# Kernel tuning notes

Measured on AMD Instinct MI355X. Metric: run time of the kernel, lower is better.

Reference implementation:

```python
import jax, jax.numpy as jnp
import numpy as np

POS_HALF = 4   # positive window: [t-4, t+4)
NEG_LEN = 12   # negatives: up to 12 frames on each side of the positive window
K_MAX = 2 * POS_HALF + 2 * NEG_LEN  # 32 candidates max per timestep


def _build_windows(T):
    """Static [T,K_MAX] gather indices + positive/valid masks (numpy, trace-time)."""
    idx = np.zeros((T, K_MAX), np.int32)
    pos_mask = np.zeros((T, K_MAX), bool)
    valid = np.zeros((T, K_MAX), bool)
    for t in range(T):
        start, end = max(0, t - POS_HALF), min(T, t + POS_HALF)
        pos = list(range(start, end))
        neg = list(range(max(0, start - NEG_LEN), start)) + \
              list(range(end, min(T, end + NEG_LEN)))
        comb = pos + neg
        idx[t, :len(comb)] = comb
        valid[t, :len(comb)] = True
        pos_mask[t, :len(pos)] = True
    return jnp.asarray(idx), jnp.asarray(pos_mask), jnp.asarray(valid)


def _directional(q, kv, idx, pos_mask, valid, scale, bias):
    # q, kv: [B,T,D] (L2-normalized); idx/pos_mask/valid: [T,K]
    w = kv[:, idx]  # [B,T,K,D] windowed gather
    logits = jnp.einsum('btd,btkd->btk', q, w) * scale + bias  # [B,T,K]
    sign = jnp.where(pos_mask, 1.0, -1.0)
    loglik = jax.nn.log_sigmoid(sign * logits)
    # per-t: sum over window, mean over batch; then sum over t
    loss = -jnp.where(valid, loglik, 0.0).sum(axis=2).mean(axis=0).sum()
    am = jnp.argmax(jnp.where(valid, logits, -jnp.inf), axis=2)  # [B,T]
    T = q.shape[1]
    correct = pos_mask[jnp.arange(T)[None, :], am].astype(jnp.float32).sum()
    return loss, correct


def setup_inputs() -> dict:
    key = jax.random.key(0)
    k1, k2 = jax.random.split(key)
    B, T, D = 8, 1024, 512
    return {
        "motion_feature": jax.random.normal(k1, (B, T, D), jnp.float32),
        "audio_feature": jax.random.normal(k2, (B, T, D), jnp.float32),
        "logit_scale": jnp.asarray(np.log(1.0 / 0.07), jnp.float32),  # param (pre-exp)
        "logit_bias": jnp.asarray(0.0, jnp.float32),                  # param
    }


def reference(motion_feature, audio_feature, logit_scale, logit_bias):
    B, T, _ = motion_feature.shape
    eps = 1e-12
    m = motion_feature / jnp.clip(
        jnp.linalg.norm(motion_feature, axis=2, keepdims=True), eps)
    a = audio_feature / jnp.clip(
        jnp.linalg.norm(audio_feature, axis=2, keepdims=True), eps)
    scale = jnp.exp(logit_scale)
    idx, pos_mask, valid = _build_windows(T)
    m2a_loss, m2a_correct = _directional(m, a, idx, pos_mask, valid, scale, logit_bias)
    a2m_loss, a2m_correct = _directional(a, m, idx, pos_mask, valid, scale, logit_bias)
    final_loss = (m2a_loss + a2m_loss) / (2 * T)
    total_correct = (m2a_correct + a2m_correct) / (2 * T * B)
    return final_loss, total_correct
```

## Files before the change

kernel.cpp:

```cpp
#include <hip/hip_runtime.h>
#include <hip/hip_bf16.h>
#include <math.h>

#define B_DIM 8
#define T_DIM 1024
#define D_DIM 512
#define BT (B_DIM * T_DIM)
#define NBLK 512

typedef __bf16 bf16x8 __attribute__((ext_vector_type(8)));
typedef float floatx4 __attribute__((ext_vector_type(4)));

__device__ __forceinline__ float wave_reduce_sum(float v) {
#pragma unroll
    for (int off = 32; off > 0; off >>= 1) v += __shfl_xor(v, off, 64);
    return v;
}

__device__ __forceinline__ float softplus(float y) {
    return fmaxf(y, 0.0f) + log1pf(expf(-fabsf(y)));
}

__device__ __forceinline__ bf16x8 cvt8(float4 x, float4 y) {
    union { ushort u[8]; bf16x8 v; } r;
    __hip_bfloat162 h0 = __float22bfloat162_rn(make_float2(x.x, x.y));
    __hip_bfloat162 h1 = __float22bfloat162_rn(make_float2(x.z, x.w));
    __hip_bfloat162 h2 = __float22bfloat162_rn(make_float2(y.x, y.y));
    __hip_bfloat162 h3 = __float22bfloat162_rn(make_float2(y.z, y.w));
    ushort2 p0 = *(ushort2*)&h0, p1 = *(ushort2*)&h1;
    ushort2 p2 = *(ushort2*)&h2, p3 = *(ushort2*)&h3;
    r.u[0] = p0.x; r.u[1] = p0.y; r.u[2] = p1.x; r.u[3] = p1.y;
    r.u[4] = p2.x; r.u[5] = p2.y; r.u[6] = p3.x; r.u[7] = p3.y;
    return r.v;
}

__global__ __launch_bounds__(512, 4) void crossband_kernel(
    const float* __restrict__ m, const float* __restrict__ a,
    const float* __restrict__ pscale, const float* __restrict__ pbias,
    float* __restrict__ part_loss, float* __restrict__ part_corr)
{
    __shared__ float red[8][5][272];
    __shared__ float Sbuf[48][49];
    __shared__ float red2[8][6][16];
    __shared__ float norms[6][16];
    __shared__ float rowpos[16], colpos[16], shl[8];

    int blk = blockIdx.x;
    int b   = blk >> 6;
    int t0  = (blk & 63) << 4;
    int tid  = threadIdx.x;
    int w    = tid >> 6;
    int lane = tid & 63;
    int mrow = lane & 15;
    int kgrp = lane >> 4;
    int koff = w * 64 + kgrp * 8;

    const float* mb = m + ((size_t)b << 19);
    const float* ab = a + ((size_t)b << 19);

    const float* mp[3]; const float* ap[3];
#pragma unroll
    for (int s = 0; s < 3; ++s) {
        int r = t0 - 16 + s * 16 + mrow;
        r = min(max(r, 0), T_DIM - 1);
        mp[s] = mb + (size_t)r * D_DIM + koff;
        ap[s] = ab + (size_t)r * D_DIM + koff;
    }

    floatx4 acc[5];
#pragma unroll
    for (int q = 0; q < 5; ++q) acc[q] = (floatx4){0.f,0.f,0.f,0.f};
    float ssm[3] = {0.f,0.f,0.f}, ssa[3] = {0.f,0.f,0.f};

#pragma unroll
    for (int ks = 0; ks < 2; ++ks) {
        bf16x8 am[3], av[3];
#pragma unroll
        for (int s = 0; s < 3; ++s) {
            float4 x = *(const float4*)(mp[s] + ks * 32);
            float4 y = *(const float4*)(mp[s] + ks * 32 + 4);
            ssm[s] += x.x*x.x + x.y*x.y + x.z*x.z + x.w*x.w
                    + y.x*y.x + y.y*y.y + y.z*y.z + y.w*y.w;
            am[s] = cvt8(x, y);
            float4 u = *(const float4*)(ap[s] + ks * 32);
            float4 v = *(const float4*)(ap[s] + ks * 32 + 4);
            ssa[s] += u.x*u.x + u.y*u.y + u.z*u.z + u.w*u.w
                    + v.x*v.x + v.y*v.y + v.z*v.z + v.w*v.w;
            av[s] = cvt8(u, v);
        }
        acc[0] = __builtin_amdgcn_mfma_f32_16x16x32_bf16(am[1], av[0], acc[0], 0, 0, 0);
        acc[1] = __builtin_amdgcn_mfma_f32_16x16x32_bf16(am[1], av[1], acc[1], 0, 0, 0);
        acc[2] = __builtin_amdgcn_mfma_f32_16x16x32_bf16(am[1], av[2], acc[2], 0, 0, 0);
        acc[3] = __builtin_amdgcn_mfma_f32_16x16x32_bf16(am[0], av[1], acc[3], 0, 0, 0);
        acc[4] = __builtin_amdgcn_mfma_f32_16x16x32_bf16(am[2], av[1], acc[4], 0, 0, 0);
    }

#pragma unroll
    for (int off = 16; off <= 32; off <<= 1) {
#pragma unroll
        for (int s = 0; s < 3; ++s) {
            ssm[s] += __shfl_xor(ssm[s], off, 64);
            ssa[s] += __shfl_xor(ssa[s], off, 64);
        }
    }
    if (kgrp == 0) {
#pragma unroll
        for (int s = 0; s < 3; ++s) {
            red2[w][s][mrow]     = ssm[s];
            red2[w][3 + s][mrow] = ssa[s];
        }
    }
#pragma unroll
    for (int q = 0; q < 5; ++q)
#pragma unroll
        for (int r = 0; r < 4; ++r)
            red[w][q][(kgrp * 4 + r) * 17 + mrow] = acc[q][r];
    __syncthreads();

    if (tid < 96) {
        int slot = tid >> 4, mr = tid & 15;
        float ss = 0.f;
#pragma unroll
        for (int ww = 0; ww < 8; ++ww) ss += red2[ww][slot][mr];
        norms[slot][mr] = 1.0f / fmaxf(sqrtf(ss), 1e-12f);
    }
    {
        const int tu[5] = {16, 16, 16, 0, 32};
        const int tv[5] = {0, 16, 32, 16, 16};
#pragma unroll
        for (int e = 0; e < 3; ++e) {
            int idx = tid + e * 512;
            if (idx < 1280) {
                int q = idx >> 8, r2 = idx & 255;
                int rho = r2 >> 4, kap = r2 & 15;
                float s4 = 0.f;
#pragma unroll
                for (int ww = 0; ww < 8; ++ww)
                    s4 += red[ww][q][rho * 17 + kap];
                Sbuf[tu[q] + rho][tv[q] + kap] = s4;
            }
        }
    }
    __syncthreads();

    float scale = expf(pscale[0]), bias = pbias[0];
    float loss = 0.0f;

    if (tid < 256) {
        int i = tid >> 4, cc = tid & 15;
        float im_u = norms[1][i];
        float mmax = -1e30f, mpos = 0.0f;
#pragma unroll
        for (int tj = 0; tj < 3; ++tj) {
            int v  = tj * 16 + cc;
            int dd = v - i;
            int c  = t0 - 16 + v;
            if (dd >= 0 && dd < 32 && c >= 0 && c < T_DIM) {
                float sv = Sbuf[16 + i][v] * norms[3 + tj][cc];
                float logit = sv * im_u * scale + bias;
                bool pos = (dd >= 12) && (dd <= 19);
                loss += softplus(pos ? -logit : logit);
                if (sv > mmax) { mmax = sv; mpos = pos ? 1.0f : 0.0f; }
            }
        }
#pragma unroll
        for (int off = 1; off < 16; off <<= 1) {
            float ov = __shfl_xor(mmax, off, 64);
            float op = __shfl_xor(mpos, off, 64);
            if (ov > mmax) { mmax = ov; mpos = op; }
        }
        if (cc == 0) rowpos[i] = mpos;
    } else {
        int t2 = tid - 256;
        int i = t2 >> 4, cc = t2 & 15;
        float ia_v = norms[4][i];
        float amax = -1e30f, apos = 0.0f;
#pragma unroll
        for (int tj = 0; tj < 3; ++tj) {
            int u2 = tj * 16 + cc;
            int ee = u2 - i;
            int r  = t0 - 16 + u2;
            if (ee >= 0 && ee < 32 && r >= 0 && r < T_DIM) {
                float sv = Sbuf[u2][16 + i] * norms[tj][cc];
                float logit = sv * ia_v * scale + bias;
                bool pos = (ee >= 12) && (ee <= 19);
                loss += softplus(pos ? -logit : logit);
                if (sv > amax) { amax = sv; apos = pos ? 1.0f : 0.0f; }
            }
        }
#pragma unroll
        for (int off = 1; off < 16; off <<= 1) {
            float ov = __shfl_xor(amax, off, 64);
            float op = __shfl_xor(apos, off, 64);
            if (ov > amax) { amax = ov; apos = op; }
        }
        if (cc == 0) colpos[i] = apos;
    }

    loss = wave_reduce_sum(loss);
    if (lane == 0) shl[w] = loss;
    __syncthreads();
    if (tid == 0) {
        float L = 0.0f, C = 0.0f;
#pragma unroll
        for (int r = 0; r < 8; ++r) L += shl[r];
#pragma unroll
        for (int r = 0; r < 16; ++r) C += rowpos[r] + colpos[r];
        part_loss[blk] = L;
        part_corr[blk] = C;
    }
}

__global__ __launch_bounds__(256) void finalsum_kernel(
    const float* __restrict__ part_loss, const float* __restrict__ part_corr,
    float* __restrict__ out)
{
    int tid = threadIdx.x;
    float l = part_loss[tid] + part_loss[tid + 256];
    float c = part_corr[tid] + part_corr[tid + 256];
    l = wave_reduce_sum(l);
    c = wave_reduce_sum(c);
    __shared__ float shl[4], shc[4];
    int w = tid >> 6, lane = tid & 63;
    if (lane == 0) { shl[w] = l; shc[w] = c; }
    __syncthreads();
    if (tid == 0) {
        out[0] = (shl[0] + shl[1] + shl[2] + shl[3]) / 16384.0f;
        out[1] = (shc[0] + shc[1] + shc[2] + shc[3]) / 16384.0f;
    }
}

extern "C" void kernel_launch(void* const* d_in, const int* in_sizes, int n_in,
                              void* d_out, int out_size, void* d_ws, size_t ws_size,
                              hipStream_t stream)
{
    const float* m  = (const float*)d_in[0];
    const float* a  = (const float*)d_in[1];
    const float* ps = (const float*)d_in[2];
    const float* pb = (const float*)d_in[3];
    float* out = (float*)d_out;

    float* part_loss = (float*)d_ws;
    float* part_corr = part_loss + NBLK;

    crossband_kernel<<<NBLK, 512, 0, stream>>>(m, a, ps, pb, part_loss, part_corr);
    finalsum_kernel<<<1, 256, 0, stream>>>(part_loss, part_corr, out);
}
```

Baseline: 90.72 us.

## Split band kernel into per-wave MFMA kernel and separate epilogue reduction kernel

The single fused kernel, where each 512-thread block reduced eight waves' partial MFMA tiles through shared memory, is replaced by two kernels. The first runs independent waves (four per 256-thread block) that write their partial dot-product tiles and squared norms to global workspace. The second kernel sums those partials, normalises, and computes the loss and argmax. Softplus also switches to fast __expf/__logf intrinsics. This trades an extra launch and about 21 MB of global partial traffic for smaller blocks and no shared-memory cross-wave reduction in the load phase.

```diff
diff --git a/kernel.cpp b/kernel.cpp
--- a/kernel.cpp
+++ b/kernel.cpp
@@ -6,7 +6,11 @@
 #define T_DIM 1024
 #define D_DIM 512
 #define BT (B_DIM * T_DIM)
-#define NBLK 512
+#define NTILES 512
+#define WPT 8
+#define NWAVES (NTILES * WPT)
+#define PART_STRIDE 1280
+#define SS_STRIDE 96
 
 typedef __bf16 bf16x8 __attribute__((ext_vector_type(8)));
 typedef float floatx4 __attribute__((ext_vector_type(4)));
@@ -18,7 +22,7 @@
 }
 
 __device__ __forceinline__ float softplus(float y) {
-    return fmaxf(y, 0.0f) + log1pf(expf(-fabsf(y)));
+    return fmaxf(y, 0.0f) + __logf(1.0f + __expf(-fabsf(y)));
 }
 
 __device__ __forceinline__ bf16x8 cvt8(float4 x, float4 y) {
@@ -34,23 +38,16 @@
     return r.v;
 }
 
-__global__ __launch_bounds__(512, 4) void crossband_kernel(
+__global__ __launch_bounds__(256, 4) void band2_kernel(
     const float* __restrict__ m, const float* __restrict__ a,
-    const float* __restrict__ pscale, const float* __restrict__ pbias,
-    float* __restrict__ part_loss, float* __restrict__ part_corr)
-{
-    __shared__ float red[8][5][272];
-    __shared__ float Sbuf[48][49];
-    __shared__ float red2[8][6][16];
-    __shared__ float norms[6][16];
-    __shared__ float rowpos[16], colpos[16], shl[8];
-
-    int blk = blockIdx.x;
-    int b   = blk >> 6;
-    int t0  = (blk & 63) << 4;
-    int tid  = threadIdx.x;
-    int w    = tid >> 6;
-    int lane = tid & 63;
+    float* __restrict__ part, float* __restrict__ ssbuf)
+{
+    int wg   = blockIdx.x * 4 + (threadIdx.x >> 6);
+    int tile = wg >> 3;
+    int w    = wg & 7;
+    int b    = tile >> 6;
+    int t0   = (tile & 63) << 4;
+    int lane = threadIdx.x & 63;
     int mrow = lane & 15;
     int kgrp = lane >> 4;
     int koff = w * 64 + kgrp * 8;
@@ -104,50 +101,65 @@
         }
     }
     if (kgrp == 0) {
+        float* sw = ssbuf + (size_t)wg * SS_STRIDE;
 #pragma unroll
         for (int s = 0; s < 3; ++s) {
-            red2[w][s][mrow]     = ssm[s];
-            red2[w][3 + s][mrow] = ssa[s];
-        }
-    }
+            sw[s * 16 + mrow]       = ssm[s];
+            sw[(3 + s) * 16 + mrow] = ssa[s];
+        }
+    }
+    float* pw = part + (size_t)wg * PART_STRIDE;
 #pragma unroll
     for (int q = 0; q < 5; ++q)
 #pragma unroll
         for (int r = 0; r < 4; ++r)
-            red[w][q][(kgrp * 4 + r) * 17 + mrow] = acc[q][r];
+            pw[q * 256 + (kgrp * 4 + r) * 16 + mrow] = acc[q][r];
+}
+
+__global__ __launch_bounds__(256) void epi_kernel(
+    const float* __restrict__ part, const float* __restrict__ ssbuf,
+    const float* __restrict__ pscale, const float* __restrict__ pbias,
+    float* __restrict__ part_loss, float* __restrict__ part_corr)
+{
+    __shared__ float Sbuf[48][49];
+    __shared__ float norms[6][16];
+    __shared__ float rowpos[16], colpos[16], shl[4];
+
+    int tile = blockIdx.x;
+    int t0   = (tile & 63) << 4;
+    int tid  = threadIdx.x;
+    int w    = tid >> 6;
+    int lane = tid & 63;
+
+    float scale = expf(pscale[0]), bias = pbias[0];
+
+    const float* pbase = part + (size_t)tile * WPT * PART_STRIDE;
+    const int tu[5] = {16, 16, 16, 0, 32};
+    const int tv[5] = {0, 16, 32, 16, 16};
+#pragma unroll
+    for (int j = 0; j < 5; ++j) {
+        int e = tid + j * 256;
+        float s = 0.f;
+#pragma unroll
+        for (int wgi = 0; wgi < WPT; ++wgi)
+            s += pbase[wgi * PART_STRIDE + e];
+        int q = e >> 8, r2 = e & 255;
+        Sbuf[tu[q] + (r2 >> 4)][tv[q] + (r2 & 15)] = s;
+    }
+    if (tid < 96) {
+        const float* sbase = ssbuf + (size_t)tile * WPT * SS_STRIDE;
+        float ss = 0.f;
+#pragma unroll
+        for (int wgi = 0; wgi < WPT; ++wgi)
+            ss += sbase[wgi * SS_STRIDE + tid];
+        norms[tid >> 4][tid & 15] = 1.0f / fmaxf(sqrtf(ss), 1e-12f);
+    }
     __syncthreads();
 
-    if (tid < 96) {
-        int slot = tid >> 4, mr = tid & 15;
-        float ss = 0.f;
-#pragma unroll
-        for (int ww = 0; ww < 8; ++ww) ss += red2[ww][slot][mr];
-        norms[slot][mr] = 1.0f / fmaxf(sqrtf(ss), 1e-12f);
-    }
+    int i = tid >> 4, cc = tid & 15;
+    float loss = 0.0f;
+
     {
-        const int tu[5] = {16, 16, 16, 0, 32};
-        const int tv[5] = {0, 16, 32, 16, 16};
-#pragma unroll
-        for (int e = 0; e < 3; ++e) {
-            int idx = tid + e * 512;
-            if (idx < 1280) {
-                int q = idx >> 8, r2 = idx & 255;
-                int rho = r2 >> 4, kap = r2 & 15;
-                float s4 = 0.f;
-#pragma unroll
-                for (int ww = 0; ww < 8; ++ww)
-                    s4 += red[ww][q][rho * 17 + kap];
-                Sbuf[tu[q] + rho][tv[q] + kap] = s4;
-            }
-        }
-    }
-    __syncthreads();
-
-    float scale = expf(pscale[0]), bias = pbias[0];
-    float loss = 0.0f;
-
-    if (tid < 256) {
-        int i = tid >> 4, cc = tid & 15;
         float im_u = norms[1][i];
         float mmax = -1e30f, mpos = 0.0f;
 #pragma unroll
@@ -170,9 +182,8 @@
             if (ov > mmax) { mmax = ov; mpos = op; }
         }
         if (cc == 0) rowpos[i] = mpos;
-    } else {
-        int t2 = tid - 256;
-        int i = t2 >> 4, cc = t2 & 15;
+    }
+    {
         float ia_v = norms[4][i];
         float amax = -1e30f, apos = 0.0f;
 #pragma unroll
@@ -201,13 +212,11 @@
     if (lane == 0) shl[w] = loss;
     __syncthreads();
     if (tid == 0) {
-        float L = 0.0f, C = 0.0f;
-#pragma unroll
-        for (int r = 0; r < 8; ++r) L += shl[r];
+        float C = 0.0f;
 #pragma unroll
         for (int r = 0; r < 16; ++r) C += rowpos[r] + colpos[r];
-        part_loss[blk] = L;
-        part_corr[blk] = C;
+        part_loss[tile] = shl[0] + shl[1] + shl[2] + shl[3];
+        part_corr[tile] = C;
     }
 }
 
@@ -240,9 +249,13 @@
     const float* pb = (const float*)d_in[3];
     float* out = (float*)d_out;
 
-    float* part_loss = (float*)d_ws;
-    float* part_corr = part_loss + NBLK;
-
-    crossband_kernel<<<NBLK, 512, 0, stream>>>(m, a, ps, pb, part_loss, part_corr);
+    float* part      = (float*)d_ws;
+    float* ssbuf     = part + (size_t)NWAVES * PART_STRIDE;
+    float* part_loss = ssbuf + (size_t)NWAVES * SS_STRIDE;
+    float* part_corr = part_loss + NTILES;
+
+    band2_kernel<<<NWAVES / 4, 256, 0, stream>>>(m, a, part, ssbuf);
+    epi_kernel<<<NTILES, 256, 0, stream>>>(part, ssbuf, ps, pb,
+                                           part_loss, part_corr);
     finalsum_kernel<<<1, 256, 0, stream>>>(part_loss, part_corr, out);
 }
```

New measurement: 98.37 us. +8.4%, slower.

## Split normalization and bf16 conversion into a prep kernel before banded MFMA

Applied to the files above, without the earlier changes.

Adds a prep kernel that L2-normalizes each row of both inputs and writes bf16 copies to workspace. The banded MFMA kernel then reads these bf16 rows, about half the bytes, and no longer computes norms, so its per-block norm reductions go away. Blocks shrink to 256 threads, each wave covering more of K, and the block order is interleaved across the batch. The cost is an extra launch plus a full fp32 read and bf16 write-then-read round trip through workspace, while the old single kernel read each fp32 row about three times from cache.

```diff
diff --git a/kernel.cpp b/kernel.cpp
--- a/kernel.cpp
+++ b/kernel.cpp
@@ -1,5 +1,4 @@
 #include <hip/hip_runtime.h>
-#include <hip/hip_bf16.h>
 #include <math.h>
 
 #define B_DIM 8
@@ -17,48 +16,67 @@
     return v;
 }
 
+__device__ __forceinline__ ushort f2bf(float x) {
+    unsigned u = __float_as_uint(x);
+    return (ushort)((u + 0x7fffu + ((u >> 16) & 1u)) >> 16);
+}
+
 __device__ __forceinline__ float softplus(float y) {
     return fmaxf(y, 0.0f) + log1pf(expf(-fabsf(y)));
 }
 
-__device__ __forceinline__ bf16x8 cvt8(float4 x, float4 y) {
-    union { ushort u[8]; bf16x8 v; } r;
-    __hip_bfloat162 h0 = __float22bfloat162_rn(make_float2(x.x, x.y));
-    __hip_bfloat162 h1 = __float22bfloat162_rn(make_float2(x.z, x.w));
-    __hip_bfloat162 h2 = __float22bfloat162_rn(make_float2(y.x, y.y));
-    __hip_bfloat162 h3 = __float22bfloat162_rn(make_float2(y.z, y.w));
-    ushort2 p0 = *(ushort2*)&h0, p1 = *(ushort2*)&h1;
-    ushort2 p2 = *(ushort2*)&h2, p3 = *(ushort2*)&h3;
-    r.u[0] = p0.x; r.u[1] = p0.y; r.u[2] = p1.x; r.u[3] = p1.y;
-    r.u[4] = p2.x; r.u[5] = p2.y; r.u[6] = p3.x; r.u[7] = p3.y;
-    return r.v;
-}
-
-__global__ __launch_bounds__(512, 4) void crossband_kernel(
+__global__ __launch_bounds__(256) void prep_kernel(
     const float* __restrict__ m, const float* __restrict__ a,
+    ushort* __restrict__ mhat, ushort* __restrict__ ahat)
+{
+    int blk = blockIdx.x;
+    int wid = (blk & 7) * 1024 + (blk >> 3) * 4 + (threadIdx.x >> 6);
+    int lane = threadIdx.x & 63;
+    const float4* mr = (const float4*)(m + (size_t)wid * D_DIM);
+    const float4* ar = (const float4*)(a + (size_t)wid * D_DIM);
+    float4 m0 = mr[lane], m1 = mr[lane + 64];
+    float4 a0 = ar[lane], a1 = ar[lane + 64];
+    float sm = m0.x*m0.x + m0.y*m0.y + m0.z*m0.z + m0.w*m0.w
+             + m1.x*m1.x + m1.y*m1.y + m1.z*m1.z + m1.w*m1.w;
+    float sa = a0.x*a0.x + a0.y*a0.y + a0.z*a0.z + a0.w*a0.w
+             + a1.x*a1.x + a1.y*a1.y + a1.z*a1.z + a1.w*a1.w;
+    sm = wave_reduce_sum(sm);
+    sa = wave_reduce_sum(sa);
+    float im = 1.0f / fmaxf(sqrtf(sm), 1e-12f);
+    float ia = 1.0f / fmaxf(sqrtf(sa), 1e-12f);
+    ushort4 mo0 = { f2bf(m0.x*im), f2bf(m0.y*im), f2bf(m0.z*im), f2bf(m0.w*im) };
+    ushort4 mo1 = { f2bf(m1.x*im), f2bf(m1.y*im), f2bf(m1.z*im), f2bf(m1.w*im) };
+    ushort4 ao0 = { f2bf(a0.x*ia), f2bf(a0.y*ia), f2bf(a0.z*ia), f2bf(a0.w*ia) };
+    ushort4 ao1 = { f2bf(a1.x*ia), f2bf(a1.y*ia), f2bf(a1.z*ia), f2bf(a1.w*ia) };
+    ushort4* mw = (ushort4*)(mhat + (size_t)wid * D_DIM);
+    ushort4* aw = (ushort4*)(ahat + (size_t)wid * D_DIM);
+    mw[lane] = mo0; mw[lane + 64] = mo1;
+    aw[lane] = ao0; aw[lane + 64] = ao1;
+}
+
+__global__ __launch_bounds__(256) void crossband_kernel(
+    const ushort* __restrict__ mhat, const ushort* __restrict__ ahat,
     const float* __restrict__ pscale, const float* __restrict__ pbias,
     float* __restrict__ part_loss, float* __restrict__ part_corr)
 {
-    __shared__ float red[8][5][272];
+    __shared__ float red[4][5][272];
     __shared__ float Sbuf[48][49];
-    __shared__ float red2[8][6][16];
-    __shared__ float norms[6][16];
-    __shared__ float rowpos[16], colpos[16], shl[8];
+    __shared__ float rowpos[16], colpos[16], shl[4];
 
     int blk = blockIdx.x;
-    int b   = blk >> 6;
-    int t0  = (blk & 63) << 4;
+    int b   = blk & 7;
+    int t0  = (blk >> 3) << 4;
     int tid  = threadIdx.x;
     int w    = tid >> 6;
     int lane = tid & 63;
     int mrow = lane & 15;
     int kgrp = lane >> 4;
-    int koff = w * 64 + kgrp * 8;
-
-    const float* mb = m + ((size_t)b << 19);
-    const float* ab = a + ((size_t)b << 19);
-
-    const float* mp[3]; const float* ap[3];
+    int koff = w * 128 + kgrp * 8;
+
+    const ushort* mb = mhat + ((size_t)b << 19);
+    const ushort* ab = ahat + ((size_t)b << 19);
+
+    const ushort* mp[3]; const ushort* ap[3];
 #pragma unroll
     for (int s = 0; s < 3; ++s) {
         int r = t0 - 16 + s * 16 + mrow;
@@ -70,23 +88,14 @@
     floatx4 acc[5];
 #pragma unroll
     for (int q = 0; q < 5; ++q) acc[q] = (floatx4){0.f,0.f,0.f,0.f};
-    float ssm[3] = {0.f,0.f,0.f}, ssa[3] = {0.f,0.f,0.f};
-
-#pragma unroll
-    for (int ks = 0; ks < 2; ++ks) {
+
+#pragma unroll
+    for (int ks = 0; ks < 4; ++ks) {
         bf16x8 am[3], av[3];
 #pragma unroll
         for (int s = 0; s < 3; ++s) {
-            float4 x = *(const float4*)(mp[s] + ks * 32);
-            float4 y = *(const float4*)(mp[s] + ks * 32 + 4);
-            ssm[s] += x.x*x.x + x.y*x.y + x.z*x.z + x.w*x.w
-                    + y.x*y.x + y.y*y.y + y.z*y.z + y.w*y.w;
-            am[s] = cvt8(x, y);
-            float4 u = *(const float4*)(ap[s] + ks * 32);
-            float4 v = *(const float4*)(ap[s] + ks * 32 + 4);
-            ssa[s] += u.x*u.x + u.y*u.y + u.z*u.z + u.w*u.w
-                    + v.x*v.x + v.y*v.y + v.z*v.z + v.w*v.w;
-            av[s] = cvt8(u, v);
+            am[s] = *(const bf16x8*)(mp[s] + ks * 32);
+            av[s] = *(const bf16x8*)(ap[s] + ks * 32);
         }
         acc[0] = __builtin_amdgcn_mfma_f32_16x16x32_bf16(am[1], av[0], acc[0], 0, 0, 0);
         acc[1] = __builtin_amdgcn_mfma_f32_16x16x32_bf16(am[1], av[1], acc[1], 0, 0, 0);
@@ -96,59 +105,32 @@
     }
 
 #pragma unroll
-    for (int off = 16; off <= 32; off <<= 1) {
-#pragma unroll
-        for (int s = 0; s < 3; ++s) {
-            ssm[s] += __shfl_xor(ssm[s], off, 64);
-            ssa[s] += __shfl_xor(ssa[s], off, 64);
-        }
-    }
-    if (kgrp == 0) {
-#pragma unroll
-        for (int s = 0; s < 3; ++s) {
-            red2[w][s][mrow]     = ssm[s];
-            red2[w][3 + s][mrow] = ssa[s];
-        }
-    }
-#pragma unroll
     for (int q = 0; q < 5; ++q)
 #pragma unroll
         for (int r = 0; r < 4; ++r)
             red[w][q][(kgrp * 4 + r) * 17 + mrow] = acc[q][r];
     __syncthreads();
 
-    if (tid < 96) {
-        int slot = tid >> 4, mr = tid & 15;
-        float ss = 0.f;
-#pragma unroll
-        for (int ww = 0; ww < 8; ++ww) ss += red2[ww][slot][mr];
-        norms[slot][mr] = 1.0f / fmaxf(sqrtf(ss), 1e-12f);
-    }
     {
         const int tu[5] = {16, 16, 16, 0, 32};
         const int tv[5] = {0, 16, 32, 16, 16};
 #pragma unroll
-        for (int e = 0; e < 3; ++e) {
-            int idx = tid + e * 512;
-            if (idx < 1280) {
-                int q = idx >> 8, r2 = idx & 255;
-                int rho = r2 >> 4, kap = r2 & 15;
-                float s4 = 0.f;
-#pragma unroll
-                for (int ww = 0; ww < 8; ++ww)
-                    s4 += red[ww][q][rho * 17 + kap];
-                Sbuf[tu[q] + rho][tv[q] + kap] = s4;
-            }
+        for (int j = 0; j < 5; ++j) {
+            int e = tid + j * 256;
+            int q = e >> 8, r2 = e & 255;
+            int rho = r2 >> 4, kap = r2 & 15;
+            float s4 = red[0][q][rho * 17 + kap] + red[1][q][rho * 17 + kap]
+                     + red[2][q][rho * 17 + kap] + red[3][q][rho * 17 + kap];
+            Sbuf[tu[q] + rho][tv[q] + kap] = s4;
         }
     }
     __syncthreads();
 
     float scale = expf(pscale[0]), bias = pbias[0];
+    int i = tid >> 4, cc = tid & 15;
     float loss = 0.0f;
 
-    if (tid < 256) {
-        int i = tid >> 4, cc = tid & 15;
-        float im_u = norms[1][i];
+    {
         float mmax = -1e30f, mpos = 0.0f;
 #pragma unroll
         for (int tj = 0; tj < 3; ++tj) {
@@ -156,8 +138,8 @@
             int dd = v - i;
             int c  = t0 - 16 + v;
             if (dd >= 0 && dd < 32 && c >= 0 && c < T_DIM) {
-                float sv = Sbuf[16 + i][v] * norms[3 + tj][cc];
-                float logit = sv * im_u * scale + bias;
+                float sv = Sbuf[16 + i][v];
+                float logit = sv * scale + bias;
                 bool pos = (dd >= 12) && (dd <= 19);
                 loss += softplus(pos ? -logit : logit);
                 if (sv > mmax) { mmax = sv; mpos = pos ? 1.0f : 0.0f; }
@@ -170,10 +152,8 @@
             if (ov > mmax) { mmax = ov; mpos = op; }
         }
         if (cc == 0) rowpos[i] = mpos;
-    } else {
-        int t2 = tid - 256;
-        int i = t2 >> 4, cc = t2 & 15;
-        float ia_v = norms[4][i];
+    }
+    {
         float amax = -1e30f, apos = 0.0f;
 #pragma unroll
         for (int tj = 0; tj < 3; ++tj) {
@@ -181,8 +161,8 @@
             int ee = u2 - i;
             int r  = t0 - 16 + u2;
             if (ee >= 0 && ee < 32 && r >= 0 && r < T_DIM) {
-                float sv = Sbuf[u2][16 + i] * norms[tj][cc];
-                float logit = sv * ia_v * scale + bias;
+                float sv = Sbuf[u2][16 + i];
+                float logit = sv * scale + bias;
                 bool pos = (ee >= 12) && (ee <= 19);
                 loss += softplus(pos ? -logit : logit);
                 if (sv > amax) { amax = sv; apos = pos ? 1.0f : 0.0f; }
@@ -201,12 +181,10 @@
     if (lane == 0) shl[w] = loss;
     __syncthreads();
     if (tid == 0) {
-        float L = 0.0f, C = 0.0f;
-#pragma unroll
-        for (int r = 0; r < 8; ++r) L += shl[r];
+        float C = 0.0f;
 #pragma unroll
         for (int r = 0; r < 16; ++r) C += rowpos[r] + colpos[r];
-        part_loss[blk] = L;
+        part_loss[blk] = shl[0] + shl[1] + shl[2] + shl[3];
         part_corr[blk] = C;
     }
 }
@@ -240,9 +218,14 @@
     const float* pb = (const float*)d_in[3];
     float* out = (float*)d_out;
 
-    float* part_loss = (float*)d_ws;
-    float* part_corr = part_loss + NBLK;
-
-    crossband_kernel<<<NBLK, 512, 0, stream>>>(m, a, ps, pb, part_loss, part_corr);
+    const size_t MHAT_ELEMS = (size_t)BT * D_DIM;
+    ushort* mhat = (ushort*)d_ws;
+    ushort* ahat = mhat + MHAT_ELEMS;
+    float*  part_loss = (float*)(ahat + MHAT_ELEMS);
+    float*  part_corr = part_loss + NBLK;
+
+    prep_kernel<<<BT / 4, 256, 0, stream>>>(m, a, mhat, ahat);
+    crossband_kernel<<<NBLK, 256, 0, stream>>>(mhat, ahat, ps, pb,
+                                               part_loss, part_corr);
     finalsum_kernel<<<1, 256, 0, stream>>>(part_loss, part_corr, out);
 }
```

After: 91.81 us. Within noise of the previous version (+1.2%).

## Split each tile into per-direction half blocks and use fast softplus intrinsics

Applied to the files above, without the earlier changes.

Each 16-row tile is now handled by two blocks, one per direction (m2a and a2m), which doubles the grid. Each block loads one center band and three neighbor bands instead of six bands and issues three MFMAs instead of five. The split raises parallelism and lowers per-block LDS and register use, with occupancy hint 6. In exchange the shared center/neighbor rows are loaded twice across the pair. Softplus switches to __logf/__expf, which is less accurate.

```diff
diff --git a/kernel.cpp b/kernel.cpp
--- a/kernel.cpp
+++ b/kernel.cpp
@@ -6,7 +6,7 @@
 #define T_DIM 1024
 #define D_DIM 512
 #define BT (B_DIM * T_DIM)
-#define NBLK 512
+#define NBLK 1024
 
 typedef __bf16 bf16x8 __attribute__((ext_vector_type(8)));
 typedef float floatx4 __attribute__((ext_vector_type(4)));
@@ -18,7 +18,7 @@
 }
 
 __device__ __forceinline__ float softplus(float y) {
-    return fmaxf(y, 0.0f) + log1pf(expf(-fabsf(y)));
+    return fmaxf(y, 0.0f) + __logf(1.0f + __expf(-fabsf(y)));
 }
 
 __device__ __forceinline__ bf16x8 cvt8(float4 x, float4 y) {
@@ -34,20 +34,23 @@
     return r.v;
 }
 
-__global__ __launch_bounds__(512, 4) void crossband_kernel(
+__global__ __launch_bounds__(512, 6) void halfband_kernel(
     const float* __restrict__ m, const float* __restrict__ a,
     const float* __restrict__ pscale, const float* __restrict__ pbias,
     float* __restrict__ part_loss, float* __restrict__ part_corr)
 {
-    __shared__ float red[8][5][272];
-    __shared__ float Sbuf[48][49];
-    __shared__ float red2[8][6][16];
-    __shared__ float norms[6][16];
-    __shared__ float rowpos[16], colpos[16], shl[8];
-
-    int blk = blockIdx.x;
-    int b   = blk >> 6;
-    int t0  = (blk & 63) << 4;
+    __shared__ float red[8][3][272];
+    __shared__ float SbufA[16][49];
+    __shared__ float SbufB[48][17];
+    __shared__ float red2[8][4][16];
+    __shared__ float norms[4][16];
+    __shared__ float qpos[16], shl[8];
+
+    int blk  = blockIdx.x;
+    int half = blk & 1;
+    int pair = blk >> 1;
+    int b    = pair >> 6;
+    int t0   = (pair & 63) << 4;
     int tid  = threadIdx.x;
     int w    = tid >> 6;
     int lane = tid & 63;
@@ -58,66 +61,62 @@
     const float* mb = m + ((size_t)b << 19);
     const float* ab = a + ((size_t)b << 19);
 
-    const float* mp[3]; const float* ap[3];
-#pragma unroll
-    for (int s = 0; s < 3; ++s) {
-        int r = t0 - 16 + s * 16 + mrow;
-        r = min(max(r, 0), T_DIM - 1);
-        mp[s] = mb + (size_t)r * D_DIM + koff;
-        ap[s] = ab + (size_t)r * D_DIM + koff;
-    }
-
-    floatx4 acc[5];
-#pragma unroll
-    for (int q = 0; q < 5; ++q) acc[q] = (floatx4){0.f,0.f,0.f,0.f};
-    float ssm[3] = {0.f,0.f,0.f}, ssa[3] = {0.f,0.f,0.f};
+    const float* ctr;
+    const float* bnd[3];
+    {
+        const float* cbase = half ? ab : mb;
+        const float* bbase = half ? mb : ab;
+        ctr = cbase + (size_t)(t0 + mrow) * D_DIM + koff;
+#pragma unroll
+        for (int s = 0; s < 3; ++s) {
+            int r = t0 - 16 + s * 16 + mrow;
+            r = min(max(r, 0), T_DIM - 1);
+            bnd[s] = bbase + (size_t)r * D_DIM + koff;
+        }
+    }
+
+    floatx4 acc[3] = {{0,0,0,0},{0,0,0,0},{0,0,0,0}};
+    float ssc = 0.f, ssb[3] = {0.f,0.f,0.f};
 
 #pragma unroll
     for (int ks = 0; ks < 2; ++ks) {
-        bf16x8 am[3], av[3];
+        float4 x = *(const float4*)(ctr + ks * 32);
+        float4 y = *(const float4*)(ctr + ks * 32 + 4);
+        ssc += x.x*x.x + x.y*x.y + x.z*x.z + x.w*x.w
+             + y.x*y.x + y.y*y.y + y.z*y.z + y.w*y.w;
+        bf16x8 cf = cvt8(x, y);
 #pragma unroll
         for (int s = 0; s < 3; ++s) {
-            float4 x = *(const float4*)(mp[s] + ks * 32);
-            float4 y = *(const float4*)(mp[s] + ks * 32 + 4);
-            ssm[s] += x.x*x.x + x.y*x.y + x.z*x.z + x.w*x.w
-                    + y.x*y.x + y.y*y.y + y.z*y.z + y.w*y.w;
-            am[s] = cvt8(x, y);
-            float4 u = *(const float4*)(ap[s] + ks * 32);
-            float4 v = *(const float4*)(ap[s] + ks * 32 + 4);
-            ssa[s] += u.x*u.x + u.y*u.y + u.z*u.z + u.w*u.w
+            float4 u = *(const float4*)(bnd[s] + ks * 32);
+            float4 v = *(const float4*)(bnd[s] + ks * 32 + 4);
+            ssb[s] += u.x*u.x + u.y*u.y + u.z*u.z + u.w*u.w
                     + v.x*v.x + v.y*v.y + v.z*v.z + v.w*v.w;
-            av[s] = cvt8(u, v);
-        }
-        acc[0] = __builtin_amdgcn_mfma_f32_16x16x32_bf16(am[1], av[0], acc[0], 0, 0, 0);
-        acc[1] = __builtin_amdgcn_mfma_f32_16x16x32_bf16(am[1], av[1], acc[1], 0, 0, 0);
-        acc[2] = __builtin_amdgcn_mfma_f32_16x16x32_bf16(am[1], av[2], acc[2], 0, 0, 0);
-        acc[3] = __builtin_amdgcn_mfma_f32_16x16x32_bf16(am[0], av[1], acc[3], 0, 0, 0);
-        acc[4] = __builtin_amdgcn_mfma_f32_16x16x32_bf16(am[2], av[1], acc[4], 0, 0, 0);
+            bf16x8 bf = cvt8(u, v);
+            acc[s] = half
+                ? __builtin_amdgcn_mfma_f32_16x16x32_bf16(bf, cf, acc[s], 0, 0, 0)
+                : __builtin_amdgcn_mfma_f32_16x16x32_bf16(cf, bf, acc[s], 0, 0, 0);
+        }
     }
 
 #pragma unroll
     for (int off = 16; off <= 32; off <<= 1) {
-#pragma unroll
-        for (int s = 0; s < 3; ++s) {
-            ssm[s] += __shfl_xor(ssm[s], off, 64);
-            ssa[s] += __shfl_xor(ssa[s], off, 64);
-        }
+        ssc += __shfl_xor(ssc, off, 64);
+#pragma unroll
+        for (int s = 0; s < 3; ++s) ssb[s] += __shfl_xor(ssb[s], off, 64);
     }
     if (kgrp == 0) {
 #pragma unroll
-        for (int s = 0; s < 3; ++s) {
-            red2[w][s][mrow]     = ssm[s];
-            red2[w][3 + s][mrow] = ssa[s];
-        }
-    }
-#pragma unroll
-    for (int q = 0; q < 5; ++q)
+        for (int s = 0; s < 3; ++s) red2[w][s][mrow] = ssb[s];
+        red2[w][3][mrow] = ssc;
+    }
+#pragma unroll
+    for (int s = 0; s < 3; ++s)
 #pragma unroll
         for (int r = 0; r < 4; ++r)
-            red[w][q][(kgrp * 4 + r) * 17 + mrow] = acc[q][r];
-    __syncthreads();
-
-    if (tid < 96) {
+            red[w][s][(kgrp * 4 + r) * 17 + mrow] = acc[s][r];
+    __syncthreads();
+
+    if (tid < 64) {
         int slot = tid >> 4, mr = tid & 15;
         float ss = 0.f;
 #pragma unroll
@@ -125,19 +124,18 @@
         norms[slot][mr] = 1.0f / fmaxf(sqrtf(ss), 1e-12f);
     }
     {
-        const int tu[5] = {16, 16, 16, 0, 32};
-        const int tv[5] = {0, 16, 32, 16, 16};
-#pragma unroll
-        for (int e = 0; e < 3; ++e) {
-            int idx = tid + e * 512;
-            if (idx < 1280) {
-                int q = idx >> 8, r2 = idx & 255;
+        int e = tid;
+#pragma unroll
+        for (int rep = 0; rep < 2; ++rep, e += 512) {
+            if (e < 768) {
+                int q = e >> 8, r2 = e & 255;
                 int rho = r2 >> 4, kap = r2 & 15;
                 float s4 = 0.f;
 #pragma unroll
                 for (int ww = 0; ww < 8; ++ww)
                     s4 += red[ww][q][rho * 17 + kap];
-                Sbuf[tu[q] + rho][tv[q] + kap] = s4;
+                if (half == 0) SbufA[rho][q * 16 + kap] = s4;
+                else           SbufB[q * 16 + rho][kap] = s4;
             }
         }
     }
@@ -148,53 +146,29 @@
 
     if (tid < 256) {
         int i = tid >> 4, cc = tid & 15;
-        float im_u = norms[1][i];
-        float mmax = -1e30f, mpos = 0.0f;
+        float inv_q = norms[3][i];
+        float qmax = -1e30f, qp = 0.0f;
 #pragma unroll
         for (int tj = 0; tj < 3; ++tj) {
-            int v  = tj * 16 + cc;
-            int dd = v - i;
-            int c  = t0 - 16 + v;
-            if (dd >= 0 && dd < 32 && c >= 0 && c < T_DIM) {
-                float sv = Sbuf[16 + i][v] * norms[3 + tj][cc];
-                float logit = sv * im_u * scale + bias;
+            int k  = tj * 16 + cc;
+            int dd = k - i;
+            int o  = t0 - 16 + k;
+            if (dd >= 0 && dd < 32 && o >= 0 && o < T_DIM) {
+                float sv = (half == 0 ? SbufA[i][k] : SbufB[k][i])
+                         * norms[tj][cc];
+                float logit = sv * inv_q * scale + bias;
                 bool pos = (dd >= 12) && (dd <= 19);
                 loss += softplus(pos ? -logit : logit);
-                if (sv > mmax) { mmax = sv; mpos = pos ? 1.0f : 0.0f; }
+                if (sv > qmax) { qmax = sv; qp = pos ? 1.0f : 0.0f; }
             }
         }
 #pragma unroll
         for (int off = 1; off < 16; off <<= 1) {
-            float ov = __shfl_xor(mmax, off, 64);
-            float op = __shfl_xor(mpos, off, 64);
-            if (ov > mmax) { mmax = ov; mpos = op; }
-        }
-        if (cc == 0) rowpos[i] = mpos;
-    } else {
-        int t2 = tid - 256;
-        int i = t2 >> 4, cc = t2 & 15;
-        float ia_v = norms[4][i];
-        float amax = -1e30f, apos = 0.0f;
-#pragma unroll
-        for (int tj = 0; tj < 3; ++tj) {
-            int u2 = tj * 16 + cc;
-            int ee = u2 - i;
-            int r  = t0 - 16 + u2;
-            if (ee >= 0 && ee < 32 && r >= 0 && r < T_DIM) {
-                float sv = Sbuf[u2][16 + i] * norms[tj][cc];
-                float logit = sv * ia_v * scale + bias;
-                bool pos = (ee >= 12) && (ee <= 19);
-                loss += softplus(pos ? -logit : logit);
-                if (sv > amax) { amax = sv; apos = pos ? 1.0f : 0.0f; }
-            }
-        }
-#pragma unroll
-        for (int off = 1; off < 16; off <<= 1) {
-            float ov = __shfl_xor(amax, off, 64);
-            float op = __shfl_xor(apos, off, 64);
-            if (ov > amax) { amax = ov; apos = op; }
-        }
-        if (cc == 0) colpos[i] = apos;
+            float ov = __shfl_xor(qmax, off, 64);
+            float op = __shfl_xor(qp, off, 64);
+            if (ov > qmax) { qmax = ov; qp = op; }
+        }
+        if (cc == 0) qpos[i] = qp;
     }
 
     loss = wave_reduce_sum(loss);
@@ -205,7 +179,7 @@
 #pragma unroll
         for (int r = 0; r < 8; ++r) L += shl[r];
 #pragma unroll
-        for (int r = 0; r < 16; ++r) C += rowpos[r] + colpos[r];
+        for (int r = 0; r < 16; ++r) C += qpos[r];
         part_loss[blk] = L;
         part_corr[blk] = C;
     }
@@ -216,8 +190,12 @@
     float* __restrict__ out)
 {
     int tid = threadIdx.x;
-    float l = part_loss[tid] + part_loss[tid + 256];
-    float c = part_corr[tid] + part_corr[tid + 256];
+    float l = 0.f, c = 0.f;
+#pragma unroll
+    for (int j = 0; j < 4; ++j) {
+        l += part_loss[tid + j * 256];
+        c += part_corr[tid + j * 256];
+    }
     l = wave_reduce_sum(l);
     c = wave_reduce_sum(c);
     __shared__ float shl[4], shc[4];
@@ -243,6 +221,7 @@
     float* part_loss = (float*)d_ws;
     float* part_corr = part_loss + NBLK;
 
-    crossband_kernel<<<NBLK, 512, 0, stream>>>(m, a, ps, pb, part_loss, part_corr);
+    halfband_kernel<<<NBLK, 512, 0, stream>>>(m, a, ps, pb,
+                                              part_loss, part_corr);
     finalsum_kernel<<<1, 256, 0, stream>>>(part_loss, part_corr, out);
 }
```

Result: slower. 118.3 us (+30.4%).
